# Performance work log

Hardware: AMD Instinct MI355X
Metric: run time of the kernel (lower is better)

Reference implementation:

```python
import jax, jax.numpy as jnp
import numpy as np

N_NODES = 100000
N_EDGES = 1600000
F_IN = 128
F_OUT = 32
HEADS = 8
ALPHA = 0.2  # LeakyReLU slope


def setup_inputs() -> dict:
    key = jax.random.key(0)
    ks = jax.random.split(key, 7)
    x = jax.random.normal(ks[0], (N_NODES, F_IN), dtype=jnp.float32)
    row = jnp.sort(jax.random.randint(ks[1], (N_EDGES,), 0, N_NODES, dtype=jnp.int32))
    col = jax.random.randint(ks[2], (N_EDGES,), 0, N_NODES, dtype=jnp.int32)
    kernels = jax.random.normal(ks[3], (HEADS, F_IN, F_OUT), dtype=jnp.float32) * 0.1
    att_self = jax.random.normal(ks[4], (HEADS, F_OUT), dtype=jnp.float32) * 0.1
    att_neigh = jax.random.normal(ks[5], (HEADS, F_OUT), dtype=jnp.float32) * 0.1
    biases = jax.random.normal(ks[6], (HEADS, F_OUT), dtype=jnp.float32) * 0.1
    return {"x": x, "row": row, "col": col, "kernels": kernels,
            "att_self": att_self, "att_neigh": att_neigh, "biases": biases}


def reference(x, row, col, kernels, att_self, att_neigh, biases):
    # GraphAttention (GAT), eval mode (dropout inactive), concat over heads.
    N = x.shape[0]
    outs = []
    for h in range(kernels.shape[0]):  # fixed small head loop
        feat = x @ kernels[h]                     # [N, F_OUT]
        a_s = feat @ att_self[h]                  # [N]
        a_n = feat @ att_neigh[h]                 # [N]
        e = a_s[row] + a_n[col]                   # [E] edge logits (SDDMM)
        e = jnp.where(e > 0, e, ALPHA * e)        # LeakyReLU(0.2)
        # row-wise (destination-node) sparse softmax, numerically stable
        m = jax.ops.segment_max(e, row, num_segments=N)
        ex = jnp.exp(e - m[row])
        denom = jax.ops.segment_sum(ex, row, num_segments=N)
        alpha = ex / denom[row]                   # [E]
        # SpMM: out[i] = sum_{e: row[e]=i} alpha[e] * feat[col[e]]
        msg = alpha[:, None] * feat[col]          # [E, F_OUT]
        out = jax.ops.segment_sum(msg, row, num_segments=N) + biases[h]
        outs.append(out)
    return jnp.concatenate(outs, axis=1)          # [N, HEADS*F_OUT]
```

## Files before the change

### kernel.cpp

```cpp
#include <hip/hip_runtime.h>
#include <hip/hip_bf16.h>
#include <math.h>


#define F_IN   128
#define F_ALL  256
#define HEADS  8
#define F_OUT  32
#define ALPHA  0.2f

using f32x4  = __attribute__((ext_vector_type(4))) float;
using bf16x8 = __attribute__((ext_vector_type(8))) short;

static __device__ __forceinline__ unsigned short f32_to_bf16(float f) {
  union { float f; unsigned u; } v; v.f = f;
  unsigned r = v.u + 0x7FFF + ((v.u >> 16) & 1);
  return (unsigned short)(r >> 16);
}
static __device__ __forceinline__ unsigned cvt_pk_bf16(float lo, float hi) {
  unsigned r;
  asm("v_cvt_pk_bf16_f32 %0, %1, %2" : "=v"(r) : "v"(lo), "v"(hi));
  return r;
}
static __device__ __forceinline__ float bf16_lo(unsigned d) {
  return __uint_as_float(d << 16);
}
static __device__ __forceinline__ float bf16_hi(unsigned d) {
  return __uint_as_float(d & 0xffff0000u);
}

__global__ __launch_bounds__(256) void prep0(const float* __restrict__ kern,
                                             const float* __restrict__ att_s,
                                             const float* __restrict__ att_n,
                                             const int* __restrict__ row,
                                             unsigned short* __restrict__ Wt,
                                             float* __restrict__ ws,
                                             float* __restrict__ wn,
                                             int* __restrict__ ptr,
                                             int N, int E) {
  int id = blockIdx.x * 256 + threadIdx.x;
  if (id < 2 * HEADS * F_IN) {
    int which = id >> 10;
    int hk = id & 1023;
    int h = hk >> 7, k = hk & 127;
    const float* att = which ? att_n : att_s;
    float s = 0.f;
#pragma unroll
    for (int f = 0; f < F_OUT; ++f)
      s += kern[(size_t)h * (F_IN * F_OUT) + k * F_OUT + f] * att[h * F_OUT + f];
    (which ? wn : ws)[hk] = s;
  } else if (id < 4096) {
    int base = (id - 2048) * 16;
#pragma unroll
    for (int i = base; i < base + 16; ++i) {
      int c = i >> 7, k = i & 127;
      Wt[i] = f32_to_bf16(kern[(size_t)(c >> 5) * (F_IN * F_OUT) + k * F_OUT + (c & 31)]);
    }
  }
  if (id <= N) {
    int lo = 0, hi = E;
    while (lo < hi) {
      int mid = (lo + hi) >> 1;
      if (row[mid] < id) lo = mid + 1; else hi = mid;
    }
    ptr[id] = lo;
  }
}

__global__ __launch_bounds__(256) void aproj_conv(const float* __restrict__ x,
                                                  const float* __restrict__ ws,
                                                  const float* __restrict__ wn,
                                                  unsigned short* __restrict__ xb,
                                                  float* __restrict__ a_s,
                                                  float* __restrict__ a_n, int N) {
  const int t = threadIdx.x;
  const int l = t & 63;
  const int o = l & 15, q = l >> 4;
  const int wid = (blockIdx.x * 256 + t) >> 6;
  const int nw  = (gridDim.x * 256) >> 6;

  const float* wrow = (o < 8 ? ws + o * F_IN : wn + (o - 8) * F_IN) + q * 32;
  float4 wv[8];
#pragma unroll
  for (int i = 0; i < 8; i++) wv[i] = reinterpret_cast<const float4*>(wrow)[i];

  for (int n = wid; n < N; n += nw) {
    const float4* xr = reinterpret_cast<const float4*>(x + (size_t)n * F_IN + q * 32);
    float acc = 0.f;
#pragma unroll
    for (int i = 0; i < 8; i++) {
      float4 xv = xr[i];
      acc += xv.x * wv[i].x + xv.y * wv[i].y + xv.z * wv[i].z + xv.w * wv[i].w;
    }
    acc += __shfl_xor(acc, 16);
    acc += __shfl_xor(acc, 32);
    if (l < 16) {
      if (o < 8) a_s[n * HEADS + o] = acc;
      else       a_n[n * HEADS + (o - 8)] = acc;
    }
    if (q == 0) {
      const float4* xc = reinterpret_cast<const float4*>(x + (size_t)n * F_IN + o * 8);
      float4 y0 = xc[0], y1 = xc[1];
      uint4 pk;
      pk.x = cvt_pk_bf16(y0.x, y0.y);
      pk.y = cvt_pk_bf16(y0.z, y0.w);
      pk.z = cvt_pk_bf16(y1.x, y1.y);
      pk.w = cvt_pk_bf16(y1.z, y1.w);
      *reinterpret_cast<uint4*>(xb + (size_t)n * F_IN + o * 8) = pk;
    }
  }
}

__global__ __launch_bounds__(256) void feat_gemm_mfma(
    const unsigned short* __restrict__ xb,
    const unsigned short* __restrict__ Wt,
    unsigned short* __restrict__ featb,
    int N) {
  const int t  = threadIdx.x;
  const int w  = t >> 6;
  const int l  = t & 63;
  const int lr = l & 15;
  const int lq = l >> 4;
  const int n0 = blockIdx.x * 64 + w * 16;

  f32x4 acc[16];
#pragma unroll
  for (int ct = 0; ct < 16; ++ct) acc[ct] = (f32x4){0.f, 0.f, 0.f, 0.f};

  int ar = n0 + lr; if (ar >= N) ar = N - 1;
  const unsigned short* xrow = xb + (size_t)ar * F_IN + lq * 8;
  bf16x8 xfr[4];
#pragma unroll
  for (int kc = 0; kc < 4; ++kc)
    xfr[kc] = *reinterpret_cast<const bf16x8*>(xrow + kc * 32);

#pragma unroll
  for (int ct = 0; ct < 16; ++ct) {
    const unsigned short* wrow = Wt + (size_t)(ct * 16 + lr) * F_IN + lq * 8;
#pragma unroll
    for (int kc = 0; kc < 4; ++kc) {
      bf16x8 wfr = *reinterpret_cast<const bf16x8*>(wrow + kc * 32);
      acc[ct] = __builtin_amdgcn_mfma_f32_16x16x32_bf16(wfr, xfr[kc], acc[ct], 0, 0, 0);
    }
  }
  if (n0 + lr < N) {
    unsigned short* frow = featb + (size_t)ar * F_ALL + lq * 4;
#pragma unroll
    for (int ct = 0; ct < 16; ++ct) {
      uint2 v;
      v.x = cvt_pk_bf16(acc[ct][0], acc[ct][1]);
      v.y = cvt_pk_bf16(acc[ct][2], acc[ct][3]);
      *reinterpret_cast<uint2*>(frow + ct * 16) = v;
    }
  }
}

__global__ __launch_bounds__(256) void gat_scatter(
    const unsigned short* __restrict__ featb,
    const float* __restrict__ a_s, const float* __restrict__ a_n,
    const int* __restrict__ col, const int* __restrict__ ptr,
    const float* __restrict__ biases, float* __restrict__ out, int N) {
  const int t  = threadIdx.x;
  const int n  = blockIdx.x * 2 + (t >> 7);
  if (n >= N) return;
  const int tl = t & 127;
  const int g  = tl >> 5;
  const int hh = (tl >> 4) & 1;
  const int h  = g * 2 + hh;
  const int s  = tl & 15;
  const int p  = s >> 3;
  const int q  = s & 7;
  const int obase = h * F_OUT + q * 4;

  const int start = ptr[n];
  const int deg   = ptr[n + 1] - start;

  if (deg == 0) {
    if (p == 0)
      *reinterpret_cast<float4*>(&out[(size_t)n * F_ALL + obase]) =
          *reinterpret_cast<const float4*>(&biases[obase]);
    return;
  }

  const float as = a_s[n * HEADS + h];
  const unsigned* fu32 = reinterpret_cast<const unsigned*>(featb);
  const size_t dbase = (size_t)h * 16 + q * 2;

  if (deg <= 32) {
    int c1 = 0, c2 = 0;
    float ex1 = 0.f, ex2 = 0.f;
    if (s < deg) {
      c1 = col[start + s];
      float v = as + a_n[c1 * HEADS + h];
      v = v > 0.f ? v : ALPHA * v;
      ex1 = __expf(v);
    }
    if (s + 16 < deg) {
      c2 = col[start + s + 16];
      float v = as + a_n[c2 * HEADS + h];
      v = v > 0.f ? v : ALPHA * v;
      ex2 = __expf(v);
    }
    float sm = ex1 + ex2;
#pragma unroll
    for (int m = 1; m <= 8; m <<= 1) sm += __shfl_xor(sm, m);
    const float inv = 1.0f / sm;

    float a0 = 0.f, a1 = 0.f, a2 = 0.f, a3 = 0.f;
    const int d1 = ((deg < 16 ? deg : 16) + 1) & ~1;
    for (int e = 0; e < d1; e += 2) {
      int   c = __shfl(c1,  e + p, 16);
      float w = __shfl(ex1, e + p, 16);
      uint2 d = *reinterpret_cast<const uint2*>(fu32 + (size_t)c * 128 + dbase);
      a0 = fmaf(w, bf16_lo(d.x), a0);
      a1 = fmaf(w, bf16_hi(d.x), a1);
      a2 = fmaf(w, bf16_lo(d.y), a2);
      a3 = fmaf(w, bf16_hi(d.y), a3);
    }
    if (deg > 16) {
      const int d2 = (deg - 16 + 1) & ~1;
      for (int e = 0; e < d2; e += 2) {
        int   c = __shfl(c2,  e + p, 16);
        float w = __shfl(ex2, e + p, 16);
        uint2 d = *reinterpret_cast<const uint2*>(fu32 + (size_t)c * 128 + dbase);
        a0 = fmaf(w, bf16_lo(d.x), a0);
        a1 = fmaf(w, bf16_hi(d.x), a1);
        a2 = fmaf(w, bf16_lo(d.y), a2);
        a3 = fmaf(w, bf16_hi(d.y), a3);
      }
    }
    a0 += __shfl_xor(a0, 8);
    a1 += __shfl_xor(a1, 8);
    a2 += __shfl_xor(a2, 8);
    a3 += __shfl_xor(a3, 8);
    if (p == 0) {
      const float4 bv = *reinterpret_cast<const float4*>(&biases[obase]);
      float4 o = {a0 * inv + bv.x, a1 * inv + bv.y, a2 * inv + bv.z, a3 * inv + bv.w};
      *reinterpret_cast<float4*>(&out[(size_t)n * F_ALL + obase]) = o;
    }
    return;
  }

  float sm = 0.f;
  for (int e = s; e < deg; e += 16) {
    int c = col[start + e];
    float v = as + a_n[c * HEADS + h];
    v = v > 0.f ? v : ALPHA * v;
    sm += __expf(v);
  }
#pragma unroll
  for (int m = 1; m <= 8; m <<= 1) sm += __shfl_xor(sm, m);
  const float inv = 1.0f / sm;

  float a0 = 0.f, a1 = 0.f, a2 = 0.f, a3 = 0.f;
  for (int e = p; e < deg; e += 2) {
    int c = col[start + e];
    float v = as + a_n[c * HEADS + h];
    v = v > 0.f ? v : ALPHA * v;
    float w = __expf(v);
    uint2 d = *reinterpret_cast<const uint2*>(fu32 + (size_t)c * 128 + dbase);
    a0 = fmaf(w, bf16_lo(d.x), a0);
    a1 = fmaf(w, bf16_hi(d.x), a1);
    a2 = fmaf(w, bf16_lo(d.y), a2);
    a3 = fmaf(w, bf16_hi(d.y), a3);
  }
  a0 += __shfl_xor(a0, 8);
  a1 += __shfl_xor(a1, 8);
  a2 += __shfl_xor(a2, 8);
  a3 += __shfl_xor(a3, 8);
  if (p == 0) {
    const float4 bv = *reinterpret_cast<const float4*>(&biases[obase]);
    float4 o = {a0 * inv + bv.x, a1 * inv + bv.y, a2 * inv + bv.z, a3 * inv + bv.w};
    *reinterpret_cast<float4*>(&out[(size_t)n * F_ALL + obase]) = o;
  }
}

extern "C" void kernel_launch(void* const* d_in, const int* in_sizes, int n_in,
                              void* d_out, int out_size, void* d_ws, size_t ws_size,
                              hipStream_t stream) {
  const float* x      = (const float*)d_in[0];
  const int*   row    = (const int*)d_in[1];
  const int*   col    = (const int*)d_in[2];
  const float* kern   = (const float*)d_in[3];
  const float* att_s  = (const float*)d_in[4];
  const float* att_n  = (const float*)d_in[5];
  const float* biases = (const float*)d_in[6];

  const int N = in_sizes[0] / F_IN;
  const int E = in_sizes[1];

  unsigned short* featb = (unsigned short*)d_ws;
  unsigned short* xb    = featb + (size_t)N * F_ALL;
  unsigned short* Wt    = xb + (size_t)N * F_IN;
  float* ws  = (float*)(Wt + F_ALL * F_IN);
  float* wn  = ws + HEADS * F_IN;
  float* a_s = wn + HEADS * F_IN;
  float* a_n = a_s + (size_t)N * HEADS;
  int*   ptr = (int*)(a_n + (size_t)N * HEADS);
  float* out = (float*)d_out;

  hipLaunchKernelGGL(prep0, dim3((N + 1 + 255) / 256), dim3(256), 0, stream,
                     kern, att_s, att_n, row, Wt, ws, wn, ptr, N, E);
  hipLaunchKernelGGL(aproj_conv, dim3(2048), dim3(256), 0, stream,
                     x, ws, wn, xb, a_s, a_n, N);
  hipLaunchKernelGGL(feat_gemm_mfma, dim3((N + 63) / 64), dim3(256), 0, stream,
                     xb, Wt, featb, N);
  hipLaunchKernelGGL(gat_scatter, dim3((N + 1) / 2), dim3(256), 0, stream,
                     featb, a_s, a_n, col, ptr, biases, out, N);
}
```

Baseline: 290.9 us.

## Use one wavefront per node in GAT scatter with single-pass softmax aggregation

The scatter kernel now assigns one 64-lane wavefront per destination node instead of 128 threads, with each lane owning 4 contiguous output features (16-byte loads per lane, 128-byte contiguous per half-wave per edge). The softmax denominator is accumulated in the same edge loop as the weighted sum, removing the separate exp pass, cross-lane reductions and final shuffle-add. Each lane recomputes the edge weight, adding redundant a_n loads and exps per edge. Edges are processed serially by all lanes, which lengthens the per-node loop but halves thread count and removes the split between even and odd edges.

```diff
diff --git a/kernel.cpp b/kernel.cpp
--- a/kernel.cpp
+++ b/kernel.cpp
@@ -161,118 +161,65 @@
     const int* __restrict__ col, const int* __restrict__ ptr,
     const float* __restrict__ biases, float* __restrict__ out, int N) {
   const int t  = threadIdx.x;
-  const int n  = blockIdx.x * 2 + (t >> 7);
+  const int n  = blockIdx.x * 4 + (t >> 6);
   if (n >= N) return;
-  const int tl = t & 127;
-  const int g  = tl >> 5;
-  const int hh = (tl >> 4) & 1;
-  const int h  = g * 2 + hh;
-  const int s  = tl & 15;
-  const int p  = s >> 3;
-  const int q  = s & 7;
-  const int obase = h * F_OUT + q * 4;
+  const int l  = t & 63;
+  const int j  = l >> 4;
+  const int q  = l & 15;
+  const int h0 = 2 * j + (q >> 3);
+  const int obase = j * 64 + q * 4;
+  const size_t dbase = (size_t)j * 32 + q * 2;
 
   const int start = ptr[n];
   const int deg   = ptr[n + 1] - start;
 
+  const float4 bv = *reinterpret_cast<const float4*>(&biases[obase]);
   if (deg == 0) {
-    if (p == 0)
-      *reinterpret_cast<float4*>(&out[(size_t)n * F_ALL + obase]) =
-          *reinterpret_cast<const float4*>(&biases[obase]);
+    *reinterpret_cast<float4*>(&out[(size_t)n * F_ALL + obase]) = bv;
     return;
   }
 
-  const float as = a_s[n * HEADS + h];
+  const float as = a_s[n * HEADS + h0];
   const unsigned* fu32 = reinterpret_cast<const unsigned*>(featb);
-  const size_t dbase = (size_t)h * 16 + q * 2;
+
+  float a0 = 0.f, a1 = 0.f, a2 = 0.f, a3 = 0.f, sm = 0.f;
 
   if (deg <= 32) {
-    int c1 = 0, c2 = 0;
-    float ex1 = 0.f, ex2 = 0.f;
-    if (s < deg) {
-      c1 = col[start + s];
-      float v = as + a_n[c1 * HEADS + h];
+    const int le = l & 31;
+    int creg = (le < deg) ? col[start + le] : 0;
+#pragma unroll 4
+    for (int e = 0; e < deg; ++e) {
+      int c = __shfl(creg, e, 32);
+      float an = a_n[c * HEADS + h0];
+      float v = as + an;
       v = v > 0.f ? v : ALPHA * v;
-      ex1 = __expf(v);
-    }
-    if (s + 16 < deg) {
-      c2 = col[start + s + 16];
-      float v = as + a_n[c2 * HEADS + h];
-      v = v > 0.f ? v : ALPHA * v;
-      ex2 = __expf(v);
-    }
-    float sm = ex1 + ex2;
-#pragma unroll
-    for (int m = 1; m <= 8; m <<= 1) sm += __shfl_xor(sm, m);
-    const float inv = 1.0f / sm;
-
-    float a0 = 0.f, a1 = 0.f, a2 = 0.f, a3 = 0.f;
-    const int d1 = ((deg < 16 ? deg : 16) + 1) & ~1;
-    for (int e = 0; e < d1; e += 2) {
-      int   c = __shfl(c1,  e + p, 16);
-      float w = __shfl(ex1, e + p, 16);
+      float w = __expf(v);
+      sm += w;
       uint2 d = *reinterpret_cast<const uint2*>(fu32 + (size_t)c * 128 + dbase);
       a0 = fmaf(w, bf16_lo(d.x), a0);
       a1 = fmaf(w, bf16_hi(d.x), a1);
       a2 = fmaf(w, bf16_lo(d.y), a2);
       a3 = fmaf(w, bf16_hi(d.y), a3);
     }
-    if (deg > 16) {
-      const int d2 = (deg - 16 + 1) & ~1;
-      for (int e = 0; e < d2; e += 2) {
-        int   c = __shfl(c2,  e + p, 16);
-        float w = __shfl(ex2, e + p, 16);
-        uint2 d = *reinterpret_cast<const uint2*>(fu32 + (size_t)c * 128 + dbase);
-        a0 = fmaf(w, bf16_lo(d.x), a0);
-        a1 = fmaf(w, bf16_hi(d.x), a1);
-        a2 = fmaf(w, bf16_lo(d.y), a2);
-        a3 = fmaf(w, bf16_hi(d.y), a3);
-      }
-    }
-    a0 += __shfl_xor(a0, 8);
-    a1 += __shfl_xor(a1, 8);
-    a2 += __shfl_xor(a2, 8);
-    a3 += __shfl_xor(a3, 8);
-    if (p == 0) {
-      const float4 bv = *reinterpret_cast<const float4*>(&biases[obase]);
-      float4 o = {a0 * inv + bv.x, a1 * inv + bv.y, a2 * inv + bv.z, a3 * inv + bv.w};
-      *reinterpret_cast<float4*>(&out[(size_t)n * F_ALL + obase]) = o;
-    }
-    return;
-  }
-
-  float sm = 0.f;
-  for (int e = s; e < deg; e += 16) {
-    int c = col[start + e];
-    float v = as + a_n[c * HEADS + h];
-    v = v > 0.f ? v : ALPHA * v;
-    sm += __expf(v);
-  }
-#pragma unroll
-  for (int m = 1; m <= 8; m <<= 1) sm += __shfl_xor(sm, m);
+  } else {
+    for (int e = 0; e < deg; ++e) {
+      int c = col[start + e];
+      float an = a_n[c * HEADS + h0];
+      float v = as + an;
+      v = v > 0.f ? v : ALPHA * v;
+      float w = __expf(v);
+      sm += w;
+      uint2 d = *reinterpret_cast<const uint2*>(fu32 + (size_t)c * 128 + dbase);
+      a0 = fmaf(w, bf16_lo(d.x), a0);
+      a1 = fmaf(w, bf16_hi(d.x), a1);
+      a2 = fmaf(w, bf16_lo(d.y), a2);
+      a3 = fmaf(w, bf16_hi(d.y), a3);
+    }
+  }
+
   const float inv = 1.0f / sm;
-
-  float a0 = 0.f, a1 = 0.f, a2 = 0.f, a3 = 0.f;
-  for (int e = p; e < deg; e += 2) {
-    int c = col[start + e];
-    float v = as + a_n[c * HEADS + h];
-    v = v > 0.f ? v : ALPHA * v;
-    float w = __expf(v);
-    uint2 d = *reinterpret_cast<const uint2*>(fu32 + (size_t)c * 128 + dbase);
-    a0 = fmaf(w, bf16_lo(d.x), a0);
-    a1 = fmaf(w, bf16_hi(d.x), a1);
-    a2 = fmaf(w, bf16_lo(d.y), a2);
-    a3 = fmaf(w, bf16_hi(d.y), a3);
-  }
-  a0 += __shfl_xor(a0, 8);
-  a1 += __shfl_xor(a1, 8);
-  a2 += __shfl_xor(a2, 8);
-  a3 += __shfl_xor(a3, 8);
-  if (p == 0) {
-    const float4 bv = *reinterpret_cast<const float4*>(&biases[obase]);
-    float4 o = {a0 * inv + bv.x, a1 * inv + bv.y, a2 * inv + bv.z, a3 * inv + bv.w};
-    *reinterpret_cast<float4*>(&out[(size_t)n * F_ALL + obase]) = o;
-  }
+  float4 o = {a0 * inv + bv.x, a1 * inv + bv.y, a2 * inv + bv.z, a3 * inv + bv.w};
+  *reinterpret_cast<float4*>(&out[(size_t)n * F_ALL + obase]) = o;
 }
 
 extern "C" void kernel_launch(void* const* d_in, const int* in_sizes, int n_in,
@@ -305,6 +252,6 @@
                      x, ws, wn, xb, a_s, a_n, N);
   hipLaunchKernelGGL(feat_gemm_mfma, dim3((N + 63) / 64), dim3(256), 0, stream,
                      xb, Wt, featb, N);
-  hipLaunchKernelGGL(gat_scatter, dim3((N + 1) / 2), dim3(256), 0, stream,
+  hipLaunchKernelGGL(gat_scatter, dim3((N + 3) / 4), dim3(256), 0, stream,
                      featb, a_s, a_n, col, ptr, biases, out, N);
 }
```

After: 271.6 us. 1.07x faster.
